# Performance work log

Hardware: AMD Instinct MI355X
Metric: run time of the kernel (lower is better)

Reference implementation:

```python
import jax, jax.numpy as jnp
import numpy as np

K = 3          # kernel size
STRIDE = 1
PAD = 1
DIL = 1


def setup_inputs() -> dict:
    key = jax.random.key(0)
    k1, k2, k3 = jax.random.split(key, 3)
    N, Cin, H, W = 8, 128, 64, 64
    Cout = 128
    x = jax.random.normal(k1, (N, Cin, H, W), dtype=jnp.float32)
    # offset channels: 2 * deformable_groups * K*K = 18, interleaved (dy, dx) per tap
    offset = jax.random.normal(k2, (N, 2 * K * K, H, W), dtype=jnp.float32)
    weight = jax.random.normal(k3, (Cout, Cin, K, K), dtype=jnp.float32) / np.sqrt(Cin * K * K)
    return {"x": x, "offset": offset, "weight": weight}


def _deform_conv(x, offset, weight):
    N, Cin, H, W = x.shape
    Cout = weight.shape[0]
    KK = K * K
    Ho, Wo = offset.shape[2], offset.shape[3]

    off = offset.reshape(N, KK, 2, Ho, Wo)
    dy = off[:, :, 0]  # [N, KK, Ho, Wo]
    dx = off[:, :, 1]

    kh = jnp.repeat(jnp.arange(K), K).astype(x.dtype)   # [KK]
    kw = jnp.tile(jnp.arange(K), K).astype(x.dtype)     # [KK]
    base_i = (jnp.arange(Ho) * STRIDE - PAD).astype(x.dtype)  # [Ho]
    base_j = (jnp.arange(Wo) * STRIDE - PAD).astype(x.dtype)  # [Wo]

    # Sampling positions: [N, KK, Ho, Wo]
    py = base_i[None, None, :, None] + (kh * DIL)[None, :, None, None] + dy
    px = base_j[None, None, None, :] + (kw * DIL)[None, :, None, None] + dx

    y0 = jnp.floor(py)
    x0 = jnp.floor(px)
    wy1 = py - y0
    wx1 = px - x0
    wy0 = 1.0 - wy1
    wx0 = 1.0 - wx1
    y0i = y0.astype(jnp.int32)
    x0i = x0.astype(jnp.int32)
    y1i = y0i + 1
    x1i = x0i + 1

    x_flat = x.reshape(N, Cin, H * W)

    def gather(yi, xi):
        # zero-padding outside the image
        mask = ((yi >= 0) & (yi < H) & (xi >= 0) & (xi < W)).astype(x.dtype)
        idx = jnp.clip(yi, 0, H - 1) * W + jnp.clip(xi, 0, W - 1)  # [N,KK,Ho,Wo]
        v = jnp.take_along_axis(x_flat, idx.reshape(N, 1, -1), axis=2)  # [N,Cin,KK*Ho*Wo]
        v = v.reshape(N, Cin, KK, Ho, Wo)
        return v * mask[:, None]

    sampled = (gather(y0i, x0i) * (wy0 * wx0)[:, None]
               + gather(y0i, x1i) * (wy0 * wx1)[:, None]
               + gather(y1i, x0i) * (wy1 * wx0)[:, None]
               + gather(y1i, x1i) * (wy1 * wx1)[:, None])  # [N,Cin,KK,Ho,Wo]

    w = weight.reshape(Cout, Cin, KK)
    return jnp.einsum('nckij,ock->noij', sampled, w)


def reference(x, offset, weight):
    return _deform_conv(x, offset, weight)
```

## Files before the change

### kernel.cpp

```cpp
#include <hip/hip_runtime.h>


#define H  64
#define W  64
#define CIN 128
#define COUT 128
#define NB 8
#define KK 9
#define SROW (CIN + 8)

typedef short bf16x8 __attribute__((ext_vector_type(8)));
typedef float f32x4  __attribute__((ext_vector_type(4)));

__device__ __forceinline__ unsigned short f2bf(float f) {
    unsigned u = __builtin_bit_cast(unsigned, f);
    u += 0x7FFFu + ((u >> 16) & 1u);
    return (unsigned short)(u >> 16);
}
__device__ __forceinline__ unsigned cvt_pk_bf16(float lo, float hi) {
    unsigned r;
    asm("v_cvt_pk_bf16_f32 %0, %1, %2" : "=v"(r) : "v"(lo), "v"(hi));
    return r;
}
__device__ __forceinline__ float lo_f(unsigned u) { return __builtin_bit_cast(float, u << 16); }
__device__ __forceinline__ float hi_f(unsigned u) { return __builtin_bit_cast(float, u & 0xFFFF0000u); }

__global__ void prep_all(const float* __restrict__ x, const float* __restrict__ w,
                         unsigned short* __restrict__ xt, unsigned short* __restrict__ wt) {
    int b = blockIdx.x;
    int t = threadIdx.x;
    if (b >= NB * H) {
        int idx = (b - NB * H) * 256 + t;
        if (idx < KK * COUT * CIN) {
            int e  = idx & 7;
            int lq = (idx >> 3) & 3;
            int lm = (idx >> 5) & 15;
            int ct = (idx >> 9) & 3;
            int nt = (idx >> 11) & 1;
            int c4 = (idx >> 12) & 3;
            int kk = idx >> 14;
            int co = (c4 << 5) + (nt << 4) + lm;
            int ch = (ct << 5) + (lq << 3) + e;
            wt[idx] = f2bf(w[(co * CIN + ch) * KK + kk]);
        }
        return;
    }
    __shared__ float tile[CIN][W + 4];
    int n = b & 7, y = b >> 3;
    const float* src = x + ((size_t)n * CIN * H + y) * W;
    #pragma unroll
    for (int it = 0; it < 8; ++it) {
        int idx = it * 256 + t;
        int c  = idx >> 4;
        int x4 = (idx & 15) << 2;
        int xs = (x4 + ((c >> 5) << 4)) & 63;
        *(float4*)&tile[c][xs] = *(const float4*)(src + (size_t)c * H * W + x4);
    }
    __syncthreads();
    int xp = t >> 2;
    int cbch = (t & 3) << 5;
    int xr = (xp + ((cbch >> 5) << 4)) & 63;
    unsigned short* dst = xt + (((size_t)(n * H + y) * W + xp) * CIN + cbch);
    unsigned rr[16];
    #pragma unroll
    for (int i = 0; i < 16; ++i)
        rr[i] = cvt_pk_bf16(tile[cbch + 2 * i][xr], tile[cbch + 2 * i + 1][xr]);
    #pragma unroll
    for (int i = 0; i < 4; ++i)
        ((uint4*)dst)[i] = make_uint4(rr[4*i], rr[4*i+1], rr[4*i+2], rr[4*i+3]);
}

struct GatherCtx {
    const unsigned short *c00, *c01, *c10, *c11;
    float w00, w01, w10, w11;
};

__device__ __forceinline__ GatherCtx gather_setup(float dy, float dx, int ho, int wo, int kk,
                                                  const unsigned short* xbase) {
    GatherCtx g;
    float py = (float)(ho - 1 + kk / 3) + dy;
    float px = (float)(wo - 1 + kk % 3) + dx;
    float y0f = floorf(py), x0f = floorf(px);
    float wy1 = py - y0f, wx1 = px - x0f;
    float wy0 = 1.f - wy1, wx0 = 1.f - wx1;
    int y0 = (int)y0f, x0 = (int)x0f;
    int y1 = y0 + 1, x1 = x0 + 1;
    bool vy0 = (unsigned)y0 < (unsigned)H, vy1 = (unsigned)y1 < (unsigned)H;
    bool vx0 = (unsigned)x0 < (unsigned)W, vx1 = (unsigned)x1 < (unsigned)W;
    g.w00 = (vy0 && vx0) ? wy0 * wx0 : 0.f;
    g.w01 = (vy0 && vx1) ? wy0 * wx1 : 0.f;
    g.w10 = (vy1 && vx0) ? wy1 * wx0 : 0.f;
    g.w11 = (vy1 && vx1) ? wy1 * wx1 : 0.f;
    int yc0 = min(max(y0, 0), H - 1), yc1 = min(max(y1, 0), H - 1);
    int xc0 = min(max(x0, 0), W - 1), xc1 = min(max(x1, 0), W - 1);
    const unsigned short* r0 = xbase + (size_t)yc0 * W * CIN;
    const unsigned short* r1 = xbase + (size_t)yc1 * W * CIN;
    g.c00 = r0 + xc0 * CIN;  g.c01 = r0 + xc1 * CIN;
    g.c10 = r1 + xc0 * CIN;  g.c11 = r1 + xc1 * CIN;
    return g;
}

__global__ __launch_bounds__(512, 4) void fused_main(
        const float* __restrict__ offs, const unsigned short* __restrict__ xt,
        const unsigned short* __restrict__ wt, unsigned short* __restrict__ S,
        float* __restrict__ out) {
    __shared__ __attribute__((aligned(16))) unsigned short samp[2][64][SROW];

    int b = blockIdx.x;
    int n = b & 7, ho = b >> 3;
    int t = threadIdx.x;
    int lane = t & 63, wv = t >> 6;
    int lm = lane & 15, lq = lane >> 4;

    int pos = t >> 3;
    int c16 = t & 7;
    int cb  = c16 << 4;

    const float* offp = offs + (size_t)n * 2 * KK * H * W + (size_t)ho * W + pos;
    const unsigned short* xb = xt + (size_t)n * H * W * CIN + cb;
    size_t srow = ((((size_t)(n * H + ho) * W + pos) * KK) << 7) + cb;

    for (int tap = 0; tap < KK; ++tap) {
        float dy = offp[(size_t)(2 * tap) * H * W];
        float dx = offp[(size_t)(2 * tap + 1) * H * W];
        GatherCtx g = gather_setup(dy, dx, ho, pos, tap, xb);
        uint4 gv[8];
        #pragma unroll
        for (int j = 0; j < 2; ++j) {
            gv[4*j+0] = *(const uint4*)(g.c00 + 8*j);
            gv[4*j+1] = *(const uint4*)(g.c01 + 8*j);
            gv[4*j+2] = *(const uint4*)(g.c10 + 8*j);
            gv[4*j+3] = *(const uint4*)(g.c11 + 8*j);
        }
        unsigned rr[8];
        #pragma unroll
        for (int j = 0; j < 2; ++j) {
            const unsigned* a0 = (const unsigned*)&gv[4*j+0];
            const unsigned* a1 = (const unsigned*)&gv[4*j+1];
            const unsigned* a2 = (const unsigned*)&gv[4*j+2];
            const unsigned* a3 = (const unsigned*)&gv[4*j+3];
            #pragma unroll
            for (int i = 0; i < 4; ++i) {
                float v0 = g.w00*lo_f(a0[i]) + g.w01*lo_f(a1[i]) + g.w10*lo_f(a2[i]) + g.w11*lo_f(a3[i]);
                float v1 = g.w00*hi_f(a0[i]) + g.w01*hi_f(a1[i]) + g.w10*hi_f(a2[i]) + g.w11*hi_f(a3[i]);
                rr[4*j+i] = cvt_pk_bf16(v0, v1);
            }
        }
        unsigned short* sp = S + srow + ((size_t)tap << 7);
        *(uint4*)(sp)     = make_uint4(rr[0], rr[1], rr[2], rr[3]);
        *(uint4*)(sp + 8) = make_uint4(rr[4], rr[5], rr[6], rr[7]);
    }
    asm volatile("s_waitcnt vmcnt(0)" ::: "memory");

    f32x4 acc[4];
    #pragma unroll
    for (int mt = 0; mt < 4; ++mt) acc[mt] = f32x4{0.f, 0.f, 0.f, 0.f};

    int slot = (lm << 2) + lq;
    const unsigned short* wvbase = wt + ((size_t)wv << 11) + (slot << 3);
    const unsigned short* sme = S + srow;

    {
        uint4 s0 = *(const uint4*)(sme);
        uint4 s1 = *(const uint4*)(sme + 8);
        unsigned short* ld = &samp[0][pos][cb];
        *(uint4*)(ld)     = s0;
        *(uint4*)(ld + 8) = s1;
    }
    __syncthreads();

    for (int tap = 0; tap < KK; ++tap) {
        uint4 nx0, nx1;
        if (tap < KK - 1) {
            const unsigned short* sr = sme + ((size_t)(tap + 1) << 7);
            nx0 = *(const uint4*)(sr);
            nx1 = *(const uint4*)(sr + 8);
        }
        const unsigned short* wkb = wvbase + ((size_t)(tap << 3) << 11);
        bf16x8 bW[4];
        #pragma unroll
        for (int ct = 0; ct < 4; ++ct)
            bW[ct] = *(const bf16x8*)(wkb + (ct << 9));

        #pragma unroll
        for (int ct = 0; ct < 4; ++ct) {
            bf16x8 a[4];
            #pragma unroll
            for (int mt = 0; mt < 4; ++mt)
                a[mt] = *(const bf16x8*)&samp[tap & 1][lm + (mt << 4)][(ct << 5) + (lq << 3)];
            #pragma unroll
            for (int mt = 0; mt < 4; ++mt)
                acc[mt] = __builtin_amdgcn_mfma_f32_16x16x32_bf16(a[mt], bW[ct], acc[mt], 0, 0, 0);
        }
        if (tap < KK - 1) {
            unsigned short* ld = &samp[(tap + 1) & 1][pos][cb];
            *(uint4*)(ld)     = nx0;
            *(uint4*)(ld + 8) = nx1;
        }
        __syncthreads();
    }

    int co = (wv << 4) + lm;
    #pragma unroll
    for (int mt = 0; mt < 4; ++mt) {
        int wob = (mt << 4) + (lq << 2);
        *(f32x4*)(out + (((size_t)(n * COUT + co) * H + ho) * W + wob)) = acc[mt];
    }
}

extern "C" void kernel_launch(void* const* d_in, const int* in_sizes, int n_in,
                              void* d_out, int out_size, void* d_ws, size_t ws_size,
                              hipStream_t stream) {
    const float* x      = (const float*)d_in[0];
    const float* offset = (const float*)d_in[1];
    const float* weight = (const float*)d_in[2];
    float* out = (float*)d_out;

    unsigned short* xt = (unsigned short*)d_ws;
    unsigned short* wt = (unsigned short*)((char*)d_ws + 8388608);
    unsigned short* S  = (unsigned short*)((char*)d_ws + 8683520);

    int wblocks = (KK * COUT * CIN + 255) / 256;
    hipLaunchKernelGGL(prep_all, dim3(NB * H + wblocks), dim3(256), 0, stream,
                       x, weight, xt, wt);
    hipLaunchKernelGGL(fused_main, dim3(NB * H), dim3(512), 0, stream,
                       offset, xt, wt, S, out);
}
```

Measured before the change: 109.3 us.

## Keep bilinear samples in registers instead of a global scratch buffer

Sampled bf16 values for all nine taps are stashed in per-thread registers rather than written to and re-read from a global workspace buffer. This removes a large global write and read round trip between the gather and MFMA phases. The next tap's LDS fill is moved ahead of the MFMA loop, and the MFMA loop runs at raised wave priority. Launch bounds are relaxed to allow the higher register use, at the cost of lower occupancy.

```diff
diff --git a/kernel.cpp b/kernel.cpp
--- a/kernel.cpp
+++ b/kernel.cpp
@@ -100,10 +100,9 @@
     return g;
 }
 
-__global__ __launch_bounds__(512, 4) void fused_main(
+__global__ __launch_bounds__(512, 2) void fused_main(
         const float* __restrict__ offs, const unsigned short* __restrict__ xt,
-        const unsigned short* __restrict__ wt, unsigned short* __restrict__ S,
-        float* __restrict__ out) {
+        const unsigned short* __restrict__ wt, float* __restrict__ out) {
     __shared__ __attribute__((aligned(16))) unsigned short samp[2][64][SROW];
 
     int b = blockIdx.x;
@@ -113,13 +112,13 @@
     int lm = lane & 15, lq = lane >> 4;
 
     int pos = t >> 3;
-    int c16 = t & 7;
-    int cb  = c16 << 4;
+    int cb  = (t & 7) << 4;
 
     const float* offp = offs + (size_t)n * 2 * KK * H * W + (size_t)ho * W + pos;
     const unsigned short* xb = xt + (size_t)n * H * W * CIN + cb;
-    size_t srow = ((((size_t)(n * H + ho) * W + pos) * KK) << 7) + cb;
-
+
+    unsigned stash[KK][8];
+    #pragma unroll
     for (int tap = 0; tap < KK; ++tap) {
         float dy = offp[(size_t)(2 * tap) * H * W];
         float dx = offp[(size_t)(2 * tap + 1) * H * W];
@@ -132,7 +131,6 @@
             gv[4*j+2] = *(const uint4*)(g.c10 + 8*j);
             gv[4*j+3] = *(const uint4*)(g.c11 + 8*j);
         }
-        unsigned rr[8];
         #pragma unroll
         for (int j = 0; j < 2; ++j) {
             const unsigned* a0 = (const unsigned*)&gv[4*j+0];
@@ -143,14 +141,10 @@
             for (int i = 0; i < 4; ++i) {
                 float v0 = g.w00*lo_f(a0[i]) + g.w01*lo_f(a1[i]) + g.w10*lo_f(a2[i]) + g.w11*lo_f(a3[i]);
                 float v1 = g.w00*hi_f(a0[i]) + g.w01*hi_f(a1[i]) + g.w10*hi_f(a2[i]) + g.w11*hi_f(a3[i]);
-                rr[4*j+i] = cvt_pk_bf16(v0, v1);
+                stash[tap][4*j+i] = cvt_pk_bf16(v0, v1);
             }
         }
-        unsigned short* sp = S + srow + ((size_t)tap << 7);
-        *(uint4*)(sp)     = make_uint4(rr[0], rr[1], rr[2], rr[3]);
-        *(uint4*)(sp + 8) = make_uint4(rr[4], rr[5], rr[6], rr[7]);
-    }
-    asm volatile("s_waitcnt vmcnt(0)" ::: "memory");
+    }
 
     f32x4 acc[4];
     #pragma unroll
@@ -158,23 +152,22 @@
 
     int slot = (lm << 2) + lq;
     const unsigned short* wvbase = wt + ((size_t)wv << 11) + (slot << 3);
-    const unsigned short* sme = S + srow;
 
     {
-        uint4 s0 = *(const uint4*)(sme);
-        uint4 s1 = *(const uint4*)(sme + 8);
         unsigned short* ld = &samp[0][pos][cb];
-        *(uint4*)(ld)     = s0;
-        *(uint4*)(ld + 8) = s1;
+        *(uint4*)(ld)     = make_uint4(stash[0][0], stash[0][1], stash[0][2], stash[0][3]);
+        *(uint4*)(ld + 8) = make_uint4(stash[0][4], stash[0][5], stash[0][6], stash[0][7]);
     }
     __syncthreads();
 
+    #pragma unroll
     for (int tap = 0; tap < KK; ++tap) {
-        uint4 nx0, nx1;
         if (tap < KK - 1) {
-            const unsigned short* sr = sme + ((size_t)(tap + 1) << 7);
-            nx0 = *(const uint4*)(sr);
-            nx1 = *(const uint4*)(sr + 8);
+            unsigned short* ld = &samp[(tap + 1) & 1][pos][cb];
+            *(uint4*)(ld)     = make_uint4(stash[tap+1][0], stash[tap+1][1],
+                                           stash[tap+1][2], stash[tap+1][3]);
+            *(uint4*)(ld + 8) = make_uint4(stash[tap+1][4], stash[tap+1][5],
+                                           stash[tap+1][6], stash[tap+1][7]);
         }
         const unsigned short* wkb = wvbase + ((size_t)(tap << 3) << 11);
         bf16x8 bW[4];
@@ -182,6 +175,7 @@
         for (int ct = 0; ct < 4; ++ct)
             bW[ct] = *(const bf16x8*)(wkb + (ct << 9));
 
+        __builtin_amdgcn_s_setprio(1);
         #pragma unroll
         for (int ct = 0; ct < 4; ++ct) {
             bf16x8 a[4];
@@ -192,11 +186,7 @@
             for (int mt = 0; mt < 4; ++mt)
                 acc[mt] = __builtin_amdgcn_mfma_f32_16x16x32_bf16(a[mt], bW[ct], acc[mt], 0, 0, 0);
         }
-        if (tap < KK - 1) {
-            unsigned short* ld = &samp[(tap + 1) & 1][pos][cb];
-            *(uint4*)(ld)     = nx0;
-            *(uint4*)(ld + 8) = nx1;
-        }
+        __builtin_amdgcn_s_setprio(0);
         __syncthreads();
     }
 
@@ -218,11 +208,10 @@
 
     unsigned short* xt = (unsigned short*)d_ws;
     unsigned short* wt = (unsigned short*)((char*)d_ws + 8388608);
-    unsigned short* S  = (unsigned short*)((char*)d_ws + 8683520);
 
     int wblocks = (KK * COUT * CIN + 255) / 256;
     hipLaunchKernelGGL(prep_all, dim3(NB * H + wblocks), dim3(256), 0, stream,
                        x, weight, xt, wt);
     hipLaunchKernelGGL(fused_main, dim3(NB * H), dim3(512), 0, stream,
-                       offset, xt, wt, S, out);
-}
+                       offset, xt, wt, out);
+}
```

After: 102.7 us. -6.0%, faster.
